# Performance work log

Measured on AMD Instinct MI355X. Metric: run time of the kernel, lower is better.

## Reference

```python
import jax, jax.numpy as jnp
import numpy as np

PARTS = [list(range(0, 17)), list(range(17, 22)), list(range(22, 27)),
         list(range(27, 36)), list(range(36, 42)), list(range(42, 48)),
         list(range(48, 68))]
NUM_PARTS = len(PARTS)
V_JOINTS = max(max(p) for p in PARTS) + 1  # 68
# joint -> part index (same as get_corr_joints)
JOINTS = np.zeros((V_JOINTS,), dtype=np.int32)
for j, part in enumerate(PARTS):
    for i in part:
        JOINTS[i] = j
BN_EPS = 1e-5


def setup_inputs() -> dict:
    key = jax.random.key(0)
    k0, k1, k2 = jax.random.split(key, 3)
    N, C, T, V = 512, 1024, 1, V_JOINTS
    x = jax.random.normal(k0, (N, C, T, V), dtype=jnp.float32)
    conv1_w = jax.random.normal(k1, (C // 4, C), dtype=jnp.float32) * 0.02  # 1x1 conv C->C/4
    conv1_b = jnp.zeros((C // 4,), dtype=jnp.float32)
    conv2_w = jax.random.normal(k2, (2,), dtype=jnp.float32) * 0.5  # 1x1 conv 2->1
    conv2_b = jnp.zeros((), dtype=jnp.float32)
    bn_gamma = jnp.ones((C,), dtype=jnp.float32)
    bn_beta = jnp.zeros((C,), dtype=jnp.float32)
    return {"x": x, "conv1_w": conv1_w, "conv1_b": conv1_b,
            "conv2_w": conv2_w, "conv2_b": conv2_b,
            "bn_gamma": bn_gamma, "bn_beta": bn_beta}


def _forward(x, conv1_w, conv1_b, conv2_w, conv2_b, bn_gamma, bn_beta):
    N, C, T, V = x.shape  # T must be 1 (required by original .view)
    joints = jnp.asarray(JOINTS)
    P = NUM_PARTS
    # part-wise mean pool over joints: (V,P) normalized one-hot
    M = jax.nn.one_hot(joints, P, dtype=x.dtype)
    M = M / jnp.sum(M, axis=0, keepdims=True)
    x_parts = jnp.einsum('nctv,vp->nctp', x, M)            # (N,C,T,P)
    # conv1: 1x1, C -> C/4
    h = jnp.einsum('nctp,oc->notp', x_parts, conv1_w) + conv1_b[None, :, None, None]
    x_cap = jnp.mean(h, axis=1, keepdims=True)             # channel avg pool
    x_cmp = jnp.max(h, axis=1, keepdims=True)              # channel max pool
    # conv2: 1x1, 2 -> 1 (cat order is (avg, max))
    att = conv2_w[0] * x_cap + conv2_w[1] * x_cmp + conv2_b  # (N,1,T,P)
    att = jnp.broadcast_to(att, (N, C, T, P)).reshape(N, C, P)
    att = jax.nn.softmax(att, axis=-1)                     # softmax over parts
    # scatter part attention back to joints
    att_j = att[:, :, joints][:, :, None, :]               # (N,C,1,V)
    y = x * att_j
    # BatchNorm2d (training mode: batch stats over N,T,V per channel)
    mean = jnp.mean(y, axis=(0, 2, 3), keepdims=True)
    var = jnp.var(y, axis=(0, 2, 3), keepdims=True)
    y_bn = (y - mean) * jax.lax.rsqrt(var + BN_EPS)
    y_bn = y_bn * bn_gamma[None, :, None, None] + bn_beta[None, :, None, None]
    return jax.nn.relu(y_bn + x)


def reference(x, conv1_w, conv1_b, conv2_w, conv2_b, bn_gamma, bn_beta):
    return _forward(x, conv1_w, conv1_b, conv2_w, conv2_b, bn_gamma, bn_beta)
```

## Files before the change

kernel.cpp:

```cpp
#include <hip/hip_runtime.h>

#define NN 512
#define CC 1024
#define OO 256
#define VV 68
#define PP 7
#define NC (NN*CC)
#define NV_CNT 34816.0f

__device__ __forceinline__ int part_of(int v){
  return (v>=17)+(v>=22)+(v>=27)+(v>=36)+(v>=42)+(v>=48);
}

__global__ __launch_bounds__(256) void k0_prep(const float* __restrict__ w1,
    float* __restrict__ w1p, float* __restrict__ accum){
  int g = blockIdx.x*256 + threadIdx.x;
  int o = g >> 8, cb = g & 255;
  float4 v = ((const float4*)w1)[g];
  ((float4*)w1p)[cb*256 + o] = v;
  if (blockIdx.x == 0){
    float4 z = make_float4(0.f,0.f,0.f,0.f);
    #pragma unroll
    for (int i=0;i<8;i++)
      ((float4*)accum)[i*256 + threadIdx.x] = z;
  }
}

__global__ __launch_bounds__(256) void k12_att(const float* __restrict__ x,
    const float* __restrict__ w1p, const float* __restrict__ b1,
    const float* __restrict__ w2, const float* __restrict__ b2,
    float* __restrict__ att, float* __restrict__ accum){
  int n = blockIdx.x;
  int t = threadIdx.x;

  __shared__ float sS[PP*1024];
  __shared__ float hred[8*256];
  __shared__ float red_s[4][PP], red_m[4][PP], pre[PP], att_s[PP];

  float qreg[4][PP];
  #pragma unroll
  for (int j=0;j<4;j++){
    int c = j*256 + t;
    const float4* xr = (const float4*)(x + ((size_t)n*CC + c)*VV);
    float s[PP];
    #pragma unroll
    for (int p=0;p<PP;p++){ s[p]=0.f; qreg[j][p]=0.f; }
    #pragma unroll
    for (int i=0;i<17;i++){
      float4 v4 = xr[i];
      #pragma unroll
      for (int jj=0;jj<4;jj++){
        int p = part_of(i*4+jj);
        float e = (jj==0)?v4.x:(jj==1)?v4.y:(jj==2)?v4.z:v4.w;
        s[p] += e;
        qreg[j][p] = fmaf(e, e, qreg[j][p]);
      }
    }
    #pragma unroll
    for (int p=0;p<PP;p++) sS[p*1024 + c] = s[p];
  }
  __syncthreads();

  int oh = t & 31, ch = t >> 5;
  float acc[8][PP];
  #pragma unroll
  for (int k=0;k<8;k++)
    #pragma unroll
    for (int p=0;p<PP;p++) acc[k][p] = 0.f;

  const float4* wp  = (const float4*)w1p;
  const float4* sf4 = (const float4*)sS;
  for (int i=0;i<32;i++){
    int gcb = ch*32 + i;
    const float4* wrow = wp + (size_t)gcb*256 + oh;
    float4 w[8];
    #pragma unroll
    for (int k=0;k<8;k++) w[k] = wrow[32*k];
    #pragma unroll
    for (int p=0;p<PP;p++){
      float4 sv = sf4[p*256 + gcb];
      #pragma unroll
      for (int k=0;k<8;k++){
        acc[k][p] = fmaf(w[k].x, sv.x, acc[k][p]);
        acc[k][p] = fmaf(w[k].y, sv.y, acc[k][p]);
        acc[k][p] = fmaf(w[k].z, sv.z, acc[k][p]);
        acc[k][p] = fmaf(w[k].w, sv.w, acc[k][p]);
      }
    }
  }

  const float inv_cnt[PP] = {1.f/17.f,1.f/5.f,1.f/5.f,1.f/9.f,1.f/6.f,1.f/6.f,1.f/20.f};
  float bo = b1[t];
  float h[PP];
  #pragma unroll
  for (int p=0;p<PP;p++){
    __syncthreads();
    #pragma unroll
    for (int k=0;k<8;k++) hred[ch*256 + k*32 + oh] = acc[k][p];
    __syncthreads();
    float hs = 0.f;
    #pragma unroll
    for (int c8=0;c8<8;c8++) hs += hred[c8*256 + t];
    h[p] = fmaf(hs, inv_cnt[p], bo);
  }

  int lane = t & 63, wid = t >> 6;
  #pragma unroll
  for (int p=0;p<PP;p++){
    float sm = h[p], mx = h[p];
    #pragma unroll
    for (int off=32; off>0; off>>=1){
      sm += __shfl_down(sm, off, 64);
      mx = fmaxf(mx, __shfl_down(mx, off, 64));
    }
    if (lane==0){ red_s[wid][p]=sm; red_m[wid][p]=mx; }
  }
  __syncthreads();
  if (t < PP){
    int p = t;
    float sm = red_s[0][p]+red_s[1][p]+red_s[2][p]+red_s[3][p];
    float mx = fmaxf(fmaxf(red_m[0][p],red_m[1][p]),
                     fmaxf(red_m[2][p],red_m[3][p]));
    pre[p] = w2[0]*(sm*(1.f/(float)OO)) + w2[1]*mx + b2[0];
  }
  __syncthreads();
  if (t == 0){
    float m = pre[0];
    #pragma unroll
    for (int p=1;p<PP;p++) m = fmaxf(m, pre[p]);
    float e[PP], sum=0.f;
    #pragma unroll
    for (int p=0;p<PP;p++){ e[p] = expf(pre[p]-m); sum += e[p]; }
    float inv = 1.f/sum;
    #pragma unroll
    for (int p=0;p<PP;p++){
      float a = e[p]*inv;
      att_s[p] = a;
      att[n*PP+p] = a;
    }
  }
  __syncthreads();

  float a[PP], a2[PP];
  #pragma unroll
  for (int p=0;p<PP;p++){ a[p] = att_s[p]; a2[p] = a[p]*a[p]; }
  float* acc_sm = accum + (n & 3)*2048;
  float* acc_sq = acc_sm + 1024;
  #pragma unroll
  for (int j=0;j<4;j++){
    int c = j*256 + t;
    float sm=0.f, sq=0.f;
    #pragma unroll
    for (int p=0;p<PP;p++){
      sm = fmaf(a[p],  sS[p*1024 + c], sm);
      sq = fmaf(a2[p], qreg[j][p],     sq);
    }
    atomicAdd(&acc_sm[c], sm);
    atomicAdd(&acc_sq[c], sq);
  }
}

__global__ __launch_bounds__(256) void k4_out(const float* __restrict__ x,
    const float* __restrict__ att, const float* __restrict__ accum,
    const float* __restrict__ gamma, const float* __restrict__ beta,
    float* __restrict__ out){
  int f = blockIdx.x*256 + threadIdx.x;
  int n = blockIdx.x / 68;
  __shared__ float s_att[PP];
  if (threadIdx.x < PP) s_att[threadIdx.x] = att[n*PP + threadIdx.x];
  __syncthreads();
  int r = f/17;
  int q = f - r*17;
  int v0 = q*4;
  int c = r & (CC-1);
  float4 xv = ((const float4*)x)[f];
  float sm = accum[c]      + accum[2048+c] + accum[4096+c] + accum[6144+c];
  float sq = accum[1024+c] + accum[3072+c] + accum[5120+c] + accum[7168+c];
  float mean = sm * (1.0f/NV_CNT);
  float var  = sq * (1.0f/NV_CNT) - mean*mean;
  float rstd = rsqrtf(var + 1e-5f);
  float sc = gamma[c]*rstd;
  float sh = beta[c] - mean*sc;
  float vals[4];
  #pragma unroll
  for (int j=0;j<4;j++){
    int p = part_of(v0 + j);
    float a = s_att[p];
    float e = (j==0)?xv.x:(j==1)?xv.y:(j==2)?xv.z:xv.w;
    vals[j] = fmaxf(fmaf(e, fmaf(a, sc, 1.0f), sh), 0.0f);
  }
  float4 ov; ov.x=vals[0]; ov.y=vals[1]; ov.z=vals[2]; ov.w=vals[3];
  ((float4*)out)[f] = ov;
}

extern "C" void kernel_launch(void* const* d_in, const int* in_sizes, int n_in,
                              void* d_out, int out_size, void* d_ws, size_t ws_size,
                              hipStream_t stream) {
  const float* x     = (const float*)d_in[0];
  const float* w1    = (const float*)d_in[1];
  const float* b1    = (const float*)d_in[2];
  const float* w2    = (const float*)d_in[3];
  const float* b2    = (const float*)d_in[4];
  const float* gamma = (const float*)d_in[5];
  const float* beta  = (const float*)d_in[6];
  float* out = (float*)d_out;

  float* w1p   = (float*)d_ws;
  float* accum = w1p + OO*CC;
  float* att   = accum + 8192;

  k0_prep <<<256,         256, 0, stream>>>(w1, w1p, accum);
  k12_att <<<NN,          256, 0, stream>>>(x, w1p, b1, w2, b2, att, accum);
  k4_out  <<<(NC*17)/256, 256, 0, stream>>>(x, att, accum, gamma, beta, out);
}
```

Measured before the change: 381.2 us.

## Stage x rows through LDS for coalesced loads and replace atomics with staged reduction

The attention kernel now loads x in coalesced float4 chunks of 128 channels into padded shared memory, instead of each thread striding through its own 272-byte row. Part sums are then computed from LDS by half the threads. Per-batch BN partial sums are written to a workspace and reduced deterministically by two small kernels, replacing global atomics. A finalize kernel precomputes scale and shift, so the output kernel no longer recomputes them per element. The trade-offs are more barriers per block, idle half-warps during the compute phase, larger shared memory use, and two extra kernel launches.

```diff
diff --git a/kernel.cpp b/kernel.cpp
--- a/kernel.cpp
+++ b/kernel.cpp
@@ -13,53 +13,61 @@
 }
 
 __global__ __launch_bounds__(256) void k0_prep(const float* __restrict__ w1,
-    float* __restrict__ w1p, float* __restrict__ accum){
+    float* __restrict__ w1p){
   int g = blockIdx.x*256 + threadIdx.x;
   int o = g >> 8, cb = g & 255;
   float4 v = ((const float4*)w1)[g];
   ((float4*)w1p)[cb*256 + o] = v;
-  if (blockIdx.x == 0){
-    float4 z = make_float4(0.f,0.f,0.f,0.f);
-    #pragma unroll
-    for (int i=0;i<8;i++)
-      ((float4*)accum)[i*256 + threadIdx.x] = z;
-  }
 }
 
 __global__ __launch_bounds__(256) void k12_att(const float* __restrict__ x,
     const float* __restrict__ w1p, const float* __restrict__ b1,
     const float* __restrict__ w2, const float* __restrict__ b2,
-    float* __restrict__ att, float* __restrict__ accum){
+    float* __restrict__ att, float* __restrict__ partial){
   int n = blockIdx.x;
   int t = threadIdx.x;
 
+  __shared__ float stg[128*69];
   __shared__ float sS[PP*1024];
-  __shared__ float hred[8*256];
   __shared__ float red_s[4][PP], red_m[4][PP], pre[PP], att_s[PP];
 
-  float qreg[4][PP];
-  #pragma unroll
-  for (int j=0;j<4;j++){
-    int c = j*256 + t;
-    const float4* xr = (const float4*)(x + ((size_t)n*CC + c)*VV);
-    float s[PP];
-    #pragma unroll
-    for (int p=0;p<PP;p++){ s[p]=0.f; qreg[j][p]=0.f; }
-    #pragma unroll
-    for (int i=0;i<17;i++){
-      float4 v4 = xr[i];
-      #pragma unroll
-      for (int jj=0;jj<4;jj++){
-        int p = part_of(i*4+jj);
-        float e = (jj==0)?v4.x:(jj==1)?v4.y:(jj==2)?v4.z:v4.w;
+  float q8[8][PP];
+  #pragma unroll
+  for (int cc=0;cc<8;cc++)
+    #pragma unroll
+    for (int p=0;p<PP;p++) q8[cc][p]=0.f;
+
+  const float4* x4 = (const float4*)x;
+  for (int cc=0; cc<8; cc++){
+    int base = n*17408 + cc*2176;
+    #pragma unroll
+    for (int k=0;k<9;k++){
+      int g = k*256 + t;
+      if (k==8 && t>=128) break;
+      float4 v = x4[base + g];
+      int row = g/17, q = g - row*17;
+      float* d = &stg[row*69 + q*4];
+      d[0]=v.x; d[1]=v.y; d[2]=v.z; d[3]=v.w;
+    }
+    __syncthreads();
+    if (t < 128){
+      const float* r = &stg[t*69];
+      int c = cc*128 + t;
+      float s[PP];
+      #pragma unroll
+      for (int p=0;p<PP;p++) s[p]=0.f;
+      #pragma unroll
+      for (int v=0; v<VV; v++){
+        int p = part_of(v);
+        float e = r[v];
         s[p] += e;
-        qreg[j][p] = fmaf(e, e, qreg[j][p]);
+        q8[cc][p] = fmaf(e, e, q8[cc][p]);
       }
-    }
-    #pragma unroll
-    for (int p=0;p<PP;p++) sS[p*1024 + c] = s[p];
-  }
-  __syncthreads();
+      #pragma unroll
+      for (int p=0;p<PP;p++) sS[p*1024 + c] = s[p];
+    }
+    __syncthreads();
+  }
 
   int oh = t & 31, ch = t >> 5;
   float acc[8][PP];
@@ -90,6 +98,7 @@
   }
 
   const float inv_cnt[PP] = {1.f/17.f,1.f/5.f,1.f/5.f,1.f/9.f,1.f/6.f,1.f/6.f,1.f/20.f};
+  float* hred = stg;
   float bo = b1[t];
   float h[PP];
   #pragma unroll
@@ -141,28 +150,59 @@
   }
   __syncthreads();
 
-  float a[PP], a2[PP];
-  #pragma unroll
-  for (int p=0;p<PP;p++){ a[p] = att_s[p]; a2[p] = a[p]*a[p]; }
-  float* acc_sm = accum + (n & 3)*2048;
-  float* acc_sq = acc_sm + 1024;
-  #pragma unroll
-  for (int j=0;j<4;j++){
-    int c = j*256 + t;
-    float sm=0.f, sq=0.f;
-    #pragma unroll
-    for (int p=0;p<PP;p++){
-      sm = fmaf(a[p],  sS[p*1024 + c], sm);
-      sq = fmaf(a2[p], qreg[j][p],     sq);
-    }
-    atomicAdd(&acc_sm[c], sm);
-    atomicAdd(&acc_sq[c], sq);
-  }
+  if (t < 128){
+    float a[PP], a2[PP];
+    #pragma unroll
+    for (int p=0;p<PP;p++){ a[p] = att_s[p]; a2[p] = a[p]*a[p]; }
+    #pragma unroll
+    for (int cc=0;cc<8;cc++){
+      int c = cc*128 + t;
+      float sm=0.f, sq=0.f;
+      #pragma unroll
+      for (int p=0;p<PP;p++){
+        sm = fmaf(a[p],  sS[p*1024 + c], sm);
+        sq = fmaf(a2[p], q8[cc][p],      sq);
+      }
+      partial[n*2048 + c]        = sm;
+      partial[n*2048 + 1024 + c] = sq;
+    }
+  }
+}
+
+__global__ __launch_bounds__(256) void k3b1_reduce(const float* __restrict__ partial,
+    float* __restrict__ p2){
+  int nch = blockIdx.x >> 2, cb = blockIdx.x & 3;
+  int c = cb*256 + threadIdx.x;
+  float sm=0.f, sq=0.f;
+  for (int i=0;i<64;i++){
+    int n = nch*64 + i;
+    sm += partial[n*2048 + c];
+    sq += partial[n*2048 + 1024 + c];
+  }
+  p2[nch*2048 + c]        = sm;
+  p2[nch*2048 + 1024 + c] = sq;
+}
+
+__global__ __launch_bounds__(256) void k3b2_finalize(const float* __restrict__ p2,
+    const float* __restrict__ gamma, const float* __restrict__ beta,
+    float* __restrict__ scsh){
+  int c = blockIdx.x*256 + threadIdx.x;
+  float sm=0.f, sq=0.f;
+  #pragma unroll
+  for (int ch=0;ch<8;ch++){
+    sm += p2[ch*2048 + c];
+    sq += p2[ch*2048 + 1024 + c];
+  }
+  float mean = sm * (1.0f/NV_CNT);
+  float var  = sq * (1.0f/NV_CNT) - mean*mean;
+  float rstd = rsqrtf(var + 1e-5f);
+  float sc = gamma[c]*rstd;
+  scsh[c]        = sc;
+  scsh[1024 + c] = beta[c] - mean*sc;
 }
 
 __global__ __launch_bounds__(256) void k4_out(const float* __restrict__ x,
-    const float* __restrict__ att, const float* __restrict__ accum,
-    const float* __restrict__ gamma, const float* __restrict__ beta,
+    const float* __restrict__ att, const float* __restrict__ scsh,
     float* __restrict__ out){
   int f = blockIdx.x*256 + threadIdx.x;
   int n = blockIdx.x / 68;
@@ -174,13 +214,8 @@
   int v0 = q*4;
   int c = r & (CC-1);
   float4 xv = ((const float4*)x)[f];
-  float sm = accum[c]      + accum[2048+c] + accum[4096+c] + accum[6144+c];
-  float sq = accum[1024+c] + accum[3072+c] + accum[5120+c] + accum[7168+c];
-  float mean = sm * (1.0f/NV_CNT);
-  float var  = sq * (1.0f/NV_CNT) - mean*mean;
-  float rstd = rsqrtf(var + 1e-5f);
-  float sc = gamma[c]*rstd;
-  float sh = beta[c] - mean*sc;
+  float sc = scsh[c];
+  float sh = scsh[1024 + c];
   float vals[4];
   #pragma unroll
   for (int j=0;j<4;j++){
@@ -205,11 +240,15 @@
   const float* beta  = (const float*)d_in[6];
   float* out = (float*)d_out;
 
-  float* w1p   = (float*)d_ws;
-  float* accum = w1p + OO*CC;
-  float* att   = accum + 8192;
-
-  k0_prep <<<256,         256, 0, stream>>>(w1, w1p, accum);
-  k12_att <<<NN,          256, 0, stream>>>(x, w1p, b1, w2, b2, att, accum);
-  k4_out  <<<(NC*17)/256, 256, 0, stream>>>(x, att, accum, gamma, beta, out);
-}
+  float* w1p     = (float*)d_ws;
+  float* partial = w1p + OO*CC;
+  float* p2      = partial + NN*2048;
+  float* scsh    = p2 + 8*2048;
+  float* att     = scsh + 2048;
+
+  k0_prep      <<<256,         256, 0, stream>>>(w1, w1p);
+  k12_att      <<<NN,          256, 0, stream>>>(x, w1p, b1, w2, b2, att, partial);
+  k3b1_reduce  <<<32,          256, 0, stream>>>(partial, p2);
+  k3b2_finalize<<<4,           256, 0, stream>>>(p2, gamma, beta, scsh);
+  k4_out       <<<(NC*17)/256, 256, 0, stream>>>(x, att, scsh, out);
+}
```

Result: faster. 344.9 us (-9.5%).
